# Kernel tuning notes

Measured on AMD Instinct MI355X. Metric: run time of the kernel, lower is better.

The kernel has to match this reference:

```python
import jax, jax.numpy as jnp
import numpy as np

H = 16      # query heads
KV = 8      # kv heads
D = 128     # head_dim
HID = 2048  # hidden_size
T = 2048    # tokens
EPS = 1e-6
THETA = 1000000.0


def setup_inputs() -> dict:
    key = jax.random.key(0)
    ks = jax.random.split(key, 4)
    return {
        "hidden_states": jax.random.normal(ks[0], (T, HID), jnp.float32),
        "positions": jnp.arange(T, dtype=jnp.int32),
        "qkv_w": jax.random.normal(ks[1], (H * D + 2 * KV * D, HID), jnp.float32) * 0.02,
        "o_w": jax.random.normal(ks[2], (HID, H * D), jnp.float32) * 0.02,
        "q_norm_w": jnp.ones((D,), jnp.float32),
        "k_norm_w": jnp.ones((D,), jnp.float32),
    }


def _rmsnorm(x, w):
    # x: [T, heads, D]; normalize over last dim
    var = jnp.mean(x * x, axis=-1, keepdims=True)
    return x * jax.lax.rsqrt(var + EPS) * w


def _rope(x, positions):
    # neox-style rotate-half; x: [T, heads, D]
    half = D // 2
    inv_freq = 1.0 / (THETA ** (jnp.arange(0, half, dtype=jnp.float32) / half * 1.0))
    inv_freq = 1.0 / (THETA ** (jnp.arange(0, D, 2, dtype=jnp.float32) / D))
    ang = positions.astype(jnp.float32)[:, None] * inv_freq  # [T, D/2]
    cos = jnp.cos(ang)[:, None, :]
    sin = jnp.sin(ang)[:, None, :]
    x1, x2 = x[..., :half], x[..., half:]
    return jnp.concatenate([x1 * cos - x2 * sin, x2 * cos + x1 * sin], axis=-1)


def reference(hidden_states, positions, qkv_w, o_w, q_norm_w, k_norm_w):
    scale = D ** -0.5
    qkv = hidden_states @ qkv_w.T  # [T, H*D + 2*KV*D]
    q = qkv[:, : H * D].reshape(T, H, D)
    k = qkv[:, H * D : H * D + KV * D].reshape(T, KV, D)
    v = qkv[:, H * D + KV * D :].reshape(T, KV, D)

    q = _rope(_rmsnorm(q, q_norm_w), positions)
    k = _rope(_rmsnorm(k, k_norm_w), positions)

    # GQA: repeat kv heads to match query heads
    rep = H // KV
    k = jnp.repeat(k, rep, axis=1)  # [T, H, D]
    v = jnp.repeat(v, rep, axis=1)

    scores = jnp.einsum("thd,shd->hts", q, k) * scale  # [H, T, T]
    causal = positions[:, None] >= positions[None, :]  # [T, T]
    scores = jnp.where(causal[None, :, :], scores, jnp.float32(-1e30))
    p = jax.nn.softmax(scores, axis=-1)
    o = jnp.einsum("hts,shd->thd", p, v).reshape(T, H * D)
    return o @ o_w.T  # [T, HID]
```

## Files before the change

kernel.cpp:

```cpp
#include <hip/hip_runtime.h>
#include <math.h>

#define T_TOK 2048
#define HID 2048
#define NH 16
#define NKV 8
#define HD 128
#define QKV_N 4096
#define EPS 1e-6f

typedef unsigned short u16;
typedef unsigned int   u32;
typedef __attribute__((ext_vector_type(8))) u16   u16x8;
typedef __attribute__((ext_vector_type(8))) short short8;
typedef __attribute__((ext_vector_type(4))) float floatx4;
typedef __attribute__((ext_vector_type(16))) float f32x16;
typedef __attribute__((ext_vector_type(4))) u32   u32x4;

__device__ __forceinline__ u16 f2bf(float x) {
    u32 u = __float_as_uint(x);
    u = (u + 0x7fffu + ((u >> 16) & 1u)) >> 16;
    return (u16)u;
}
__device__ __forceinline__ float bf2f(u16 h) {
    return __uint_as_float(((u32)h) << 16);
}
__device__ __forceinline__ u32 cvtpk_bf16(float lo, float hi) {
    u32 r;
    asm("v_cvt_pk_bf16_f32 %0, %1, %2" : "=v"(r) : "v"(lo), "v"(hi));
    return r;
}

__device__ __forceinline__ void cvt8(const float* __restrict__ in,
                                     u16* __restrict__ out, size_t i)
{
    float4 a = *(const float4*)(in + i);
    float4 b = *(const float4*)(in + i + 4);
    u16x8 o;
    o[0] = f2bf(a.x); o[1] = f2bf(a.y); o[2] = f2bf(a.z); o[3] = f2bf(a.w);
    o[4] = f2bf(b.x); o[5] = f2bf(b.y); o[6] = f2bf(b.z); o[7] = f2bf(b.w);
    *(u16x8*)(out + i) = o;
}

__global__ __launch_bounds__(256) void cvt_pair(
    const float* __restrict__ ina, u16* __restrict__ outa,
    const float* __restrict__ inb, u16* __restrict__ outb)
{
    const int bid = blockIdx.x;
    if (bid < 2048) cvt8(ina, outa, ((size_t)bid * 256 + threadIdx.x) * 8);
    else            cvt8(inb, outb, ((size_t)(bid - 2048) * 256 + threadIdx.x) * 8);
}

__global__ __launch_bounds__(256) void addf32(
    float* __restrict__ out, const float* __restrict__ part)
{
    const size_t i = ((size_t)blockIdx.x * 256 + threadIdx.x) * 8;
    float4 a0 = *(const float4*)(out + i);
    float4 a1 = *(const float4*)(out + i + 4);
    float4 b0 = *(const float4*)(part + i);
    float4 b1 = *(const float4*)(part + i + 4);
    a0.x += b0.x; a0.y += b0.y; a0.z += b0.z; a0.w += b0.w;
    a1.x += b1.x; a1.y += b1.y; a1.z += b1.z; a1.w += b1.w;
    *(float4*)(out + i)     = a0;
    *(float4*)(out + i + 4) = a1;
}

#define GBM 256
#define GBN 128
#define GBK 64
#define BUFSH 24576

#define WAITV6 asm volatile("s_waitcnt vmcnt(6)" ::: "memory")
#define WAITV0 asm volatile("s_waitcnt vmcnt(0)" ::: "memory")
#define LGKM0  asm volatile("s_waitcnt lgkmcnt(0)" ::: "memory")
#define BARR   asm volatile("s_barrier" ::: "memory")
#define SB     __builtin_amdgcn_sched_barrier(0)

#define STAGEU(i, tt, dstb) \
    __builtin_amdgcn_global_load_lds( \
        (const __attribute__((address_space(1))) u32*)(gsrc[i] + (size_t)(tt)*GBK), \
        (__attribute__((address_space(3))) u32*)((dstb) + loff[i]), 16, 0, 0)

#define RD_A(dst, srcb, f) do { \
    dst[0] = *(const short8*)((srcb) + arow + (f)*1024 + achunk0); \
    dst[1] = *(const short8*)((srcb) + arow + (f)*1024 + achunk1); } while (0)

#define RD_B(dst, srcb) do { \
    _Pragma("unroll") \
    for (int j_ = 0; j_ < 4; ++j_) { \
        dst[j_][0] = *(const short8*)((srcb) + 16384 + brow + j_*1024 + achunk0); \
        dst[j_][1] = *(const short8*)((srcb) + 16384 + brow + j_*1024 + achunk1); } } while (0)

#define MM(f, aa, bb) do { \
    __builtin_amdgcn_s_setprio(1); \
    _Pragma("unroll") \
    for (int j_ = 0; j_ < 4; ++j_) { \
        acc[f][j_] = __builtin_amdgcn_mfma_f32_16x16x32_bf16(aa[0], bb[j_][0], acc[f][j_], 0, 0, 0); \
        acc[f][j_] = __builtin_amdgcn_mfma_f32_16x16x32_bf16(aa[1], bb[j_][1], acc[f][j_], 0, 0, 0); } \
    __builtin_amdgcn_s_setprio(0); } while (0)

#define TILE(t, CURB, NXTB, THDB, BBC, BBN) do { \
    const bool st_ = (t) + 2 < nt; \
    if (st_) { STAGEU(0, (t)+2, THDB); STAGEU(1, (t)+2, THDB); } \
    RD_A(aP1, CURB, 1); SB; \
    MM(0, aP0, BBC); SB; \
    if (st_) { STAGEU(2, (t)+2, THDB); STAGEU(3, (t)+2, THDB); } \
    RD_A(aP0, CURB, 2); SB; \
    MM(1, aP1, BBC); SB; \
    if (st_) { STAGEU(4, (t)+2, THDB); STAGEU(5, (t)+2, THDB); } \
    RD_A(aP1, CURB, 3); SB; \
    MM(2, aP0, BBC); \
    if ((t) + 1 < nt) { \
        if (st_) { WAITV6; } else { WAITV0; } \
        LGKM0; BARR; SB; \
        RD_B(BBN, NXTB); RD_A(aP0, NXTB, 0); \
    } \
    SB; \
    MM(3, aP1, BBC); SB; \
} while (0)

template<bool OUT_BF16>
__global__ __launch_bounds__(512, 2) void gemm_bt_8p(
    const u16* __restrict__ A, const u16* __restrict__ B,
    void* __restrict__ Cv, void* __restrict__ Cv2,
    int Ks, int lda, int ldb, int ldc)
{
    extern __shared__ short lds[];
    const int tid = threadIdx.x;
    const int w  = tid >> 6;
    const int l  = tid & 63;
    const int m0 = blockIdx.y * GBM;
    const int n0 = blockIdx.x * GBN;
    const int z  = blockIdx.z;
    A += (size_t)z * Ks;
    B += (size_t)z * Ks;
    void* Cw = z ? Cv2 : Cv;
    const int mr = (w >> 1) * 64;
    const int nc = (w & 1) * 64;
    const int cc = l & 15;
    const int q4 = l >> 4;

    const int lr = l >> 3;
    const int gchunk = ((l & 7) ^ (lr & 7)) * 8;
    const u16* gsrc[6]; int loff[6];
    #pragma unroll
    for (int i = 0; i < 6; ++i) {
        const int u = w * 6 + i;
        if (u < 32) {
            gsrc[i] = A + (size_t)(m0 + u*8 + lr) * lda + gchunk;
            loff[i] = u * 512;
        } else {
            const int v = u - 32;
            gsrc[i] = B + (size_t)(n0 + v*8 + lr) * ldb + gchunk;
            loff[i] = 16384 + v * 512;
        }
    }

    const int achunk0 = ((q4)     ^ (cc & 7)) * 8;
    const int achunk1 = ((4 + q4) ^ (cc & 7)) * 8;
    const int arow = (mr + cc) * 64;
    const int brow = (nc + cc) * 64;

    floatx4 acc[4][4];
    #pragma unroll
    for (int f = 0; f < 4; ++f)
        #pragma unroll
        for (int j = 0; j < 4; ++j) acc[f][j] = (floatx4){0.f, 0.f, 0.f, 0.f};

    short8 aP0[2], aP1[2], bbE[4][2], bbO[4][2];
    short* b0 = lds;
    short* b1 = lds + BUFSH;
    short* b2 = lds + 2 * BUFSH;
    const int nt = Ks >> 6;

    #pragma unroll
    for (int i = 0; i < 6; ++i) STAGEU(i, 0, b0);
    #pragma unroll
    for (int i = 0; i < 6; ++i) STAGEU(i, 1, b1);
    WAITV6; BARR; SB;
    RD_B(bbE, b0); RD_A(aP0, b0, 0);

    short *CURB = b0, *NXTB = b1, *THDB = b2;
    for (int t = 0; t < nt; t += 2) {
        TILE(t, CURB, NXTB, THDB, bbE, bbO);
        { short* tmp = CURB; CURB = NXTB; NXTB = THDB; THDB = tmp; }
        TILE(t + 1, CURB, NXTB, THDB, bbO, bbE);
        { short* tmp = CURB; CURB = NXTB; NXTB = THDB; THDB = tmp; }
    }

    const int r0 = q4 * 4;
    #pragma unroll
    for (int f = 0; f < 4; ++f)
        #pragma unroll
        for (int j = 0; j < 4; ++j)
            #pragma unroll
            for (int r = 0; r < 4; ++r) {
                const int row = m0 + mr + f*16 + r0 + r;
                const int col = n0 + nc + j*16 + cc;
                if (OUT_BF16)
                    ((u16*)Cw)[(size_t)row * ldc + col] = f2bf(acc[f][j][r]);
                else
                    ((float*)Cw)[(size_t)row * ldc + col] = acc[f][j][r];
            }
}

__global__ __launch_bounds__(256) void prep_cvt(
    u16* __restrict__ qkv, const int* __restrict__ positions,
    const float* __restrict__ qw, const float* __restrict__ kw,
    u16* __restrict__ Kp, u16* __restrict__ Vtp,
    const float* __restrict__ ow, u16* __restrict__ owbf)
{
    const int bid = blockIdx.x;
    if (bid >= 256) {
        cvt8(ow, owbf, ((size_t)(bid - 256) * 256 + threadIdx.x) * 8);
        return;
    }
    const int tile = bid & 31, kvh = bid >> 5;
    const int tid = threadIdx.x;
    const int w = tid >> 6, l = tid & 63;
    const int t0 = tile * 64;

    const float qw0 = qw[2*l], qw1 = qw[2*l+1];
    const float kw0 = kw[2*l], kw1 = kw[2*l+1];
    const int   i0  = (2*l) & 63;
    const float if0 = exp2f(-(float)i0     * 0.311430758895690f);
    const float if1 = exp2f(-(float)(i0+1) * 0.311430758895690f);

    for (int rr = w; rr < 64; rr += 4) {
        const int t = t0 + rr;
        const int pos = positions[t];
        const float a0 = (float)pos * if0;
        const float a1 = (float)pos * if1;
        const float s0 = sinf(a0), c0 = cosf(a0);
        const float s1 = sinf(a1), c1 = cosf(a1);

        #pragma unroll
        for (int pass = 0; pass < 3; ++pass) {
            const int off = (pass < 2) ? (2*kvh + pass)*HD : NH*HD + kvh*HD;
            const float w0 = (pass < 2) ? qw0 : kw0;
            const float w1 = (pass < 2) ? qw1 : kw1;
            u16* p = qkv + (size_t)t*QKV_N + off;

            const u32 pk = *(const u32*)(p + 2*l);
            const float x0 = bf2f((u16)pk), x1 = bf2f((u16)(pk >> 16));
            float ss = x0*x0 + x1*x1;
            #pragma unroll
            for (int x = 1; x < 64; x <<= 1) ss += __shfl_xor(ss, x);
            const float rs = rsqrtf(ss * (1.0f/128.0f) + EPS);
            const float xn0 = x0 * rs * w0, xn1 = x1 * rs * w1;
            const float px0 = __shfl_xor(xn0, 32);
            const float px1 = __shfl_xor(xn1, 32);

            float o0, o1;
            if (l < 32) { o0 = xn0*c0 - px0*s0; o1 = xn1*c1 - px1*s1; }
            else        { o0 = xn0*c0 + px0*s0; o1 = xn1*c1 + px1*s1; }
            const u32 outpk = (u32)f2bf(o0) | ((u32)f2bf(o1) << 16);

            if (pass < 2) {
                *(u32*)(p + 2*l) = outpk;
            } else {
                const int ch = l >> 2;
                u16* dst = Kp + ((size_t)(kvh*32 + tile)*64 + rr)*128
                              + (ch ^ (rr & 15))*8 + (l & 3)*2;
                *(u32*)dst = outpk;
            }
        }
    }

    __shared__ u16 tl[64][136];
    {
        const int t  = tid >> 2;
        const int c0 = (tid & 3) * 32;
        const u16* src = qkv + (size_t)(t0 + t)*QKV_N + NH*HD + NKV*HD + kvh*HD + c0;
        #pragma unroll
        for (int p2 = 0; p2 < 4; ++p2)
            *(u16x8*)(&tl[t][c0 + p2*8]) = *(const u16x8*)(src + p2*8);
    }
    __syncthreads();
    {
        u16* dstb = Vtp + (size_t)(kvh*32 + tile) * 128 * 64;
        #pragma unroll
        for (int i = 0; i < 4; ++i) {
            const int id = tid*4 + i;
            const int d = id >> 3;
            const int o = id & 7;
            const int sb = (o ^ (d & 7)) * 8;
            u16x8 v;
            #pragma unroll
            for (int j = 0; j < 8; ++j) v[j] = tl[sb + j][d];
            *(u16x8*)(dstb + d*64 + o*8) = v;
        }
    }
}

__global__ __launch_bounds__(256, 2) void attn_mfma32(
    const u16* __restrict__ qkv, const u16* __restrict__ Kp,
    const u16* __restrict__ Vtp,
    u16* __restrict__ Opart, float2* __restrict__ ml)
{
    const int id   = blockIdx.x;
    const int kvh  = id & 7;
    const int u    = id >> 3;
    const int half = u >> 5;
    const int v    = u & 31;
    const int hp   = v & 1;
    const int bq   = v >> 1;
    const int qt   = half ? bq : 15 - bq;
    const int h    = kvh*2 + hp;
    const int t0q  = qt * 128;

    const int tid = threadIdx.x;
    const int w   = tid >> 6;
    const int l   = tid & 63;
    const int q31 = l & 31;
    const int hi  = l >> 5;

    __shared__ short Ks[2][8192];
    __shared__ short Vts[2][8192];

    short8 qf[8];
    {
        const u16* qrow = qkv + (size_t)(t0q + w*32 + q31) * QKV_N + h*HD;
        #pragma unroll
        for (int ks = 0; ks < 8; ++ks)
            qf[ks] = *(const short8*)(qrow + ks*16 + hi*8);
    }

    float m_run = -3.0e38f, l_run = 0.f;
    f32x16 accO[4];
    #pragma unroll
    for (int nd = 0; nd < 4; ++nd)
        #pragma unroll
        for (int r = 0; r < 16; ++r) accO[nd][r] = 0.f;

    const float Cs = 0.12751744f;

    const int nt  = 2*qt + 2;
    const int nh0 = qt + 1;
    const int tlo = half ? nh0 : 0;
    const int thi = half ? nt  : nh0;

    auto issue = [&](int tile, int buf) {
        const size_t tb = (size_t)(kvh*32 + tile) * 8192;
        const u16* g = ((w < 2) ? Kp : Vtp) + tb + (w & 1)*4096 + l*8;
        short* p = ((w < 2) ? Ks[buf] : Vts[buf]) + (w & 1)*4096 + l*8;
        #pragma unroll
        for (int i = 0; i < 8; ++i)
            __builtin_amdgcn_global_load_lds(
                (const __attribute__((address_space(1))) u32*)(g + i*512),
                (__attribute__((address_space(3))) u32*)(p + i*512), 16, 0, 0);
    };

    issue(tlo, 0);
    int cur = 0;

    for (int tile = tlo; tile < thi; ++tile) {
        __syncthreads();
        if (tile + 1 < thi) issue(tile + 1, cur ^ 1);

        const short* Kc = Ks[cur];
        const short* Vc = Vts[cur];

        f32x16 accS0, accS1;
        #pragma unroll
        for (int r = 0; r < 16; ++r) { accS0[r] = 0.f; accS1[r] = 0.f; }

        __builtin_amdgcn_s_setprio(1);
        #pragma unroll
        for (int ks = 0; ks < 8; ++ks) {
            const int pc = ((2*ks + hi) ^ (q31 & 15)) * 8;
            short8 a0 = *(const short8*)(Kc + q31*128 + pc);
            short8 a1 = *(const short8*)(Kc + (32 + q31)*128 + pc);
            accS0 = __builtin_amdgcn_mfma_f32_32x32x16_bf16(a0, qf[ks], accS0, 0, 0, 0);
            accS1 = __builtin_amdgcn_mfma_f32_32x32x16_bf16(a1, qf[ks], accS1, 0, 0, 0);
        }
        __builtin_amdgcn_s_setprio(0);

        if (tile >= 2*qt) {
            const int qg = w*32 + q31 + t0q - tile*64;
            #pragma unroll
            for (int r = 0; r < 16; ++r) {
                const int kvb = (r&3) + 8*(r>>2) + (hi<<2);
                if (kvb > qg)      accS0[r] = -1.0e30f;
                if (kvb + 32 > qg) accS1[r] = -1.0e30f;
            }
        }

        float mx = accS0[0];
        #pragma unroll
        for (int r = 1; r < 16; ++r) mx = fmaxf(mx, accS0[r]);
        #pragma unroll
        for (int r = 0; r < 16; ++r) mx = fmaxf(mx, accS1[r]);
        mx = fmaxf(mx, __shfl_xor(mx, 32));

        if (__any(mx > m_run + 11.76f)) {
            const float m_new = fmaxf(m_run, mx);
            const float alpha = exp2f((m_run - m_new) * Cs);
            l_run *= alpha;
            m_run = m_new;
            #pragma unroll
            for (int r = 0; r < 16; ++r) {
                const float ar = __shfl(alpha, ((r&3) + 8*(r>>2)) + (hi<<2));
                accO[0][r] *= ar; accO[1][r] *= ar;
                accO[2][r] *= ar; accO[3][r] *= ar;
            }
        }

        const float mb = m_run * Cs;
        float lsum = 0.f;
        #pragma unroll
        for (int r = 0; r < 16; ++r) {
            const float e0 = exp2f(accS0[r]*Cs - mb);
            const float e1 = exp2f(accS1[r]*Cs - mb);
            accS0[r] = e0; accS1[r] = e1;
            lsum += e0 + e1;
        }
        lsum += __shfl_xor(lsum, 32);
        l_run += lsum;

        __builtin_amdgcn_s_setprio(1);
        #pragma unroll
        for (int ks = 0; ks < 4; ++ks) {
            const int R = (ks & 1) * 8;
            u32 x0, x1, x2, x3;
            if (ks < 2) {
                x0 = cvtpk_bf16(accS0[R+0], accS0[R+1]);
                x1 = cvtpk_bf16(accS0[R+2], accS0[R+3]);
                x2 = cvtpk_bf16(accS0[R+4], accS0[R+5]);
                x3 = cvtpk_bf16(accS0[R+6], accS0[R+7]);
            } else {
                x0 = cvtpk_bf16(accS1[R+0], accS1[R+1]);
                x1 = cvtpk_bf16(accS1[R+2], accS1[R+3]);
                x2 = cvtpk_bf16(accS1[R+4], accS1[R+5]);
                x3 = cvtpk_bf16(accS1[R+6], accS1[R+7]);
            }
            asm("v_permlane32_swap_b32 %0, %1" : "+v"(x0), "+v"(x2));
            asm("v_permlane32_swap_b32 %0, %1" : "+v"(x1), "+v"(x3));
            u32x4 aw; aw.x = x0; aw.y = x1; aw.z = x2; aw.w = x3;
            const short8 aP = __builtin_bit_cast(short8, aw);
            #pragma unroll
            for (int nd = 0; nd < 4; ++nd) {
                short8 bv = *(const short8*)(Vc + (nd*32 + q31)*64
                                             + ((2*ks + hi) ^ (q31 & 7))*8);
                accO[nd] = __builtin_amdgcn_mfma_f32_32x32x16_bf16(aP, bv, accO[nd], 0, 0, 0);
            }
        }
        __builtin_amdgcn_s_setprio(0);

        cur ^= 1;
    }

    const size_t pbase = (size_t)(half * NH + h) * T_TOK;
    #pragma unroll
    for (int r = 0; r < 16; ++r) {
        const int qr = (r&3) + 8*(r>>2) + (hi<<2);
        u16* op = Opart + (pbase + t0q + w*32 + qr) * HD;
        op[q31]      = f2bf(accO[0][r]);
        op[32 + q31] = f2bf(accO[1][r]);
        op[64 + q31] = f2bf(accO[2][r]);
        op[96 + q31] = f2bf(accO[3][r]);
    }
    if (l < 32)
        ml[pbase + t0q + w*32 + l] = make_float2(m_run, l_run);
}

__global__ __launch_bounds__(256) void attn_combine(
    const u16* __restrict__ Opart, const float2* __restrict__ ml,
    u16* __restrict__ qkv)
{
    const int idx = blockIdx.x * 256 + threadIdx.x;
    const int c16 = idx & 15;
    const int t   = (idx >> 4) & (T_TOK - 1);
    const int h   = idx >> 15;
    const size_t iA = (size_t)h * T_TOK + t;
    const size_t iB = (size_t)(NH + h) * T_TOK + t;
    const float2 a = ml[iA];
    const float2 b = ml[iB];
    const float Cs = 0.12751744f;
    const float mM = fmaxf(a.x, b.x);
    const float wA = exp2f((a.x - mM) * Cs);
    const float wB = exp2f((b.x - mM) * Cs);
    const float inv = 1.0f / (wA * a.y + wB * b.y);
    const u16x8 A = *(const u16x8*)(Opart + iA * HD + c16*8);
    const u16x8 B = *(const u16x8*)(Opart + iB * HD + c16*8);
    u16x8 o;
    #pragma unroll
    for (int j = 0; j < 8; ++j)
        o[j] = f2bf((wA * bf2f(A[j]) + wB * bf2f(B[j])) * inv);
    *(u16x8*)(qkv + (size_t)t * QKV_N + h * HD + c16*8) = o;
}

extern "C" void kernel_launch(void* const* d_in, const int* in_sizes, int n_in,
                              void* d_out, int out_size, void* d_ws, size_t ws_size,
                              hipStream_t stream)
{
    const float* hidden    = (const float*)d_in[0];
    const int*   positions = (const int*)  d_in[1];
    const float* qkv_w     = (const float*)d_in[2];
    const float* o_w       = (const float*)d_in[3];
    const float* q_norm_w  = (const float*)d_in[4];
    const float* k_norm_w  = (const float*)d_in[5];
    float* out = (float*)d_out;

    u16* qkvbf = (u16*)d_ws;
    u16* wbf   = qkvbf + (size_t)T_TOK * QKV_N;
    u16* abf   = wbf   + (size_t)QKV_N * HID;
    u16* kpb   = abf   + (size_t)T_TOK * HID;
    u16* vpb   = kpb   + (size_t)NKV * T_TOK * HD;
    float* partC = (float*)wbf;

    static bool s_attr = false;
    if (!s_attr) {
        (void)hipFuncSetAttribute(
            reinterpret_cast<const void*>(&gemm_bt_8p<true>),
            hipFuncAttributeMaxDynamicSharedMemorySize, 147456);
        (void)hipFuncSetAttribute(
            reinterpret_cast<const void*>(&gemm_bt_8p<false>),
            hipFuncAttributeMaxDynamicSharedMemorySize, 147456);
        s_attr = true;
    }

    cvt_pair<<<6144, 256, 0, stream>>>(hidden, abf, qkv_w, wbf);

    gemm_bt_8p<true><<<dim3(QKV_N/GBN, T_TOK/GBM, 1), 512, 147456, stream>>>(
        abf, wbf, qkvbf, qkvbf, HID, HID, HID, QKV_N);

    prep_cvt<<<2304, 256, 0, stream>>>(
        qkvbf, positions, q_norm_w, k_norm_w, kpb, vpb, o_w, abf);

    attn_mfma32<<<512, 256, 0, stream>>>(qkvbf, kpb, vpb, wbf, (float2*)out);

    attn_combine<<<(NH*T_TOK*16)/256, 256, 0, stream>>>(
        wbf, (const float2*)out, qkvbf);

    gemm_bt_8p<false><<<dim3(HID/GBN, T_TOK/GBM, 2), 512, 147456, stream>>>(
        qkvbf, abf, out, partC, HID/2, QKV_N, HID, HID);

    addf32<<<(T_TOK*HID)/2048, 256, 0, stream>>>(out, partC);
}
```

Before: 244.5 us.

## Split attention KV range four ways with 512-thread blocks and move o_w conversion

```diff
diff --git a/kernel.cpp b/kernel.cpp
--- a/kernel.cpp
+++ b/kernel.cpp
@@ -204,17 +204,12 @@
             }
 }
 
-__global__ __launch_bounds__(256) void prep_cvt(
+__global__ __launch_bounds__(256) void prep(
     u16* __restrict__ qkv, const int* __restrict__ positions,
     const float* __restrict__ qw, const float* __restrict__ kw,
-    u16* __restrict__ Kp, u16* __restrict__ Vtp,
-    const float* __restrict__ ow, u16* __restrict__ owbf)
+    u16* __restrict__ Kp, u16* __restrict__ Vtp)
 {
     const int bid = blockIdx.x;
-    if (bid >= 256) {
-        cvt8(ow, owbf, ((size_t)(bid - 256) * 256 + threadIdx.x) * 8);
-        return;
-    }
     const int tile = bid & 31, kvh = bid >> 5;
     const int tid = threadIdx.x;
     const int w = tid >> 6, l = tid & 63;
@@ -293,21 +288,23 @@
     }
 }
 
-__global__ __launch_bounds__(256, 2) void attn_mfma32(
+__global__ __launch_bounds__(512, 4) void attn_mfma32(
     const u16* __restrict__ qkv, const u16* __restrict__ Kp,
     const u16* __restrict__ Vtp,
-    u16* __restrict__ Opart, float2* __restrict__ ml)
-{
-    const int id   = blockIdx.x;
-    const int kvh  = id & 7;
-    const int u    = id >> 3;
-    const int half = u >> 5;
-    const int v    = u & 31;
-    const int hp   = v & 1;
-    const int bq   = v >> 1;
-    const int qt   = half ? bq : 15 - bq;
-    const int h    = kvh*2 + hp;
-    const int t0q  = qt * 128;
+    u16* __restrict__ P0, u16* __restrict__ P1,
+    u16* __restrict__ P2, u16* __restrict__ P3,
+    float2* __restrict__ ml)
+{
+    const int id  = blockIdx.x;
+    const int kvh = id & 7;
+    const int u   = id >> 3;
+    const int hp  = u & 1;
+    const int p   = (u >> 1) & 3;
+    const int q3  = (u >> 3) & 3;
+    const int top = u >> 5;
+    const int qt  = top ? 7 - q3 : q3;
+    const int h   = kvh*2 + hp;
+    const int t0q = qt * 256;
 
     const int tid = threadIdx.x;
     const int w   = tid >> 6;
@@ -335,20 +332,19 @@
 
     const float Cs = 0.12751744f;
 
-    const int nt  = 2*qt + 2;
-    const int nh0 = qt + 1;
-    const int tlo = half ? nh0 : 0;
-    const int thi = half ? nt  : nh0;
+    const int nt  = 4*qt + 4;
+    const int tlo = p * (qt + 1);
+    const int thi = tlo + (qt + 1);
 
     auto issue = [&](int tile, int buf) {
         const size_t tb = (size_t)(kvh*32 + tile) * 8192;
-        const u16* g = ((w < 2) ? Kp : Vtp) + tb + (w & 1)*4096 + l*8;
-        short* p = ((w < 2) ? Ks[buf] : Vts[buf]) + (w & 1)*4096 + l*8;
-        #pragma unroll
-        for (int i = 0; i < 8; ++i)
+        const u16* g = ((w < 4) ? Kp : Vtp) + tb + (w & 3)*2048 + l*8;
+        short* pl = ((w < 4) ? Ks[buf] : Vts[buf]) + (w & 3)*2048 + l*8;
+        #pragma unroll
+        for (int i = 0; i < 4; ++i)
             __builtin_amdgcn_global_load_lds(
                 (const __attribute__((address_space(1))) u32*)(g + i*512),
-                (__attribute__((address_space(3))) u32*)(p + i*512), 16, 0, 0);
+                (__attribute__((address_space(3))) u32*)(pl + i*512), 16, 0, 0);
     };
 
     issue(tlo, 0);
@@ -376,13 +372,14 @@
         }
         __builtin_amdgcn_s_setprio(0);
 
-        if (tile >= 2*qt) {
-            const int qg = w*32 + q31 + t0q - tile*64;
+        if (tile >= 4*qt) {
+            const int qg   = t0q + w*32 + q31;
+            const int kvb0 = tile*64 + (hi << 2);
             #pragma unroll
             for (int r = 0; r < 16; ++r) {
-                const int kvb = (r&3) + 8*(r>>2) + (hi<<2);
-                if (kvb > qg)      accS0[r] = -1.0e30f;
-                if (kvb + 32 > qg) accS1[r] = -1.0e30f;
+                const int kvg = kvb0 + (r&3) + 8*(r>>2);
+                if (kvg > qg)      accS0[r] = -1.0e30f;
+                if (kvg + 32 > qg) accS1[r] = -1.0e30f;
             }
         }
 
@@ -450,43 +447,58 @@
         cur ^= 1;
     }
 
-    const size_t pbase = (size_t)(half * NH + h) * T_TOK;
+    u16* Op = (p == 0) ? P0 : (p == 1) ? P1 : (p == 2) ? P2 : P3;
+    const size_t hb = (size_t)h * T_TOK;
     #pragma unroll
     for (int r = 0; r < 16; ++r) {
         const int qr = (r&3) + 8*(r>>2) + (hi<<2);
-        u16* op = Opart + (pbase + t0q + w*32 + qr) * HD;
+        u16* op = Op + (hb + t0q + w*32 + qr) * HD;
         op[q31]      = f2bf(accO[0][r]);
         op[32 + q31] = f2bf(accO[1][r]);
         op[64 + q31] = f2bf(accO[2][r]);
         op[96 + q31] = f2bf(accO[3][r]);
     }
     if (l < 32)
-        ml[pbase + t0q + w*32 + l] = make_float2(m_run, l_run);
-}
-
-__global__ __launch_bounds__(256) void attn_combine(
-    const u16* __restrict__ Opart, const float2* __restrict__ ml,
-    u16* __restrict__ qkv)
-{
-    const int idx = blockIdx.x * 256 + threadIdx.x;
+        ml[(size_t)p*NH*T_TOK + hb + t0q + w*32 + l]
+            = make_float2(m_run, l_run);
+}
+
+__global__ __launch_bounds__(256) void combine4_cvt(
+    const u16* __restrict__ P0, const u16* __restrict__ P1,
+    const u16* __restrict__ P2, const u16* __restrict__ P3,
+    const float2* __restrict__ ml, u16* __restrict__ qkv,
+    const float* __restrict__ ow, u16* __restrict__ owbf)
+{
+    const int bid = blockIdx.x;
+    if (bid >= 2048) {
+        cvt8(ow, owbf, ((size_t)(bid - 2048) * 256 + threadIdx.x) * 8);
+        return;
+    }
+    const int idx = bid * 256 + threadIdx.x;
     const int c16 = idx & 15;
     const int t   = (idx >> 4) & (T_TOK - 1);
     const int h   = idx >> 15;
-    const size_t iA = (size_t)h * T_TOK + t;
-    const size_t iB = (size_t)(NH + h) * T_TOK + t;
-    const float2 a = ml[iA];
-    const float2 b = ml[iB];
+    const size_t base = (size_t)h * T_TOK + t;
+    const size_t NT = (size_t)NH * T_TOK;
+    const float2 a = ml[base];
+    const float2 b = ml[base + NT];
+    const float2 c = ml[base + 2*NT];
+    const float2 d = ml[base + 3*NT];
     const float Cs = 0.12751744f;
-    const float mM = fmaxf(a.x, b.x);
+    const float mM = fmaxf(fmaxf(a.x, b.x), fmaxf(c.x, d.x));
     const float wA = exp2f((a.x - mM) * Cs);
     const float wB = exp2f((b.x - mM) * Cs);
-    const float inv = 1.0f / (wA * a.y + wB * b.y);
-    const u16x8 A = *(const u16x8*)(Opart + iA * HD + c16*8);
-    const u16x8 B = *(const u16x8*)(Opart + iB * HD + c16*8);
+    const float wC = exp2f((c.x - mM) * Cs);
+    const float wD = exp2f((d.x - mM) * Cs);
+    const float inv = 1.0f / (wA*a.y + wB*b.y + wC*c.y + wD*d.y);
+    const u16x8 A = *(const u16x8*)(P0 + base * HD + c16*8);
+    const u16x8 B = *(const u16x8*)(P1 + base * HD + c16*8);
+    const u16x8 C = *(const u16x8*)(P2 + base * HD + c16*8);
+    const u16x8 D = *(const u16x8*)(P3 + base * HD + c16*8);
     u16x8 o;
     #pragma unroll
     for (int j = 0; j < 8; ++j)
-        o[j] = f2bf((wA * bf2f(A[j]) + wB * bf2f(B[j])) * inv);
+        o[j] = f2bf((wA*bf2f(A[j]) + wB*bf2f(B[j]) + wC*bf2f(C[j]) + wD*bf2f(D[j])) * inv);
     *(u16x8*)(qkv + (size_t)t * QKV_N + h * HD + c16*8) = o;
 }
 
@@ -507,6 +519,12 @@
     u16* abf   = wbf   + (size_t)QKV_N * HID;
     u16* kpb   = abf   + (size_t)T_TOK * HID;
     u16* vpb   = kpb   + (size_t)NKV * T_TOK * HD;
+
+    u16* P0 = wbf;
+    u16* P1 = wbf + (size_t)NH * T_TOK * HD;
+    u16* P2 = abf;
+    u16* P3 = (u16*)out;
+    float2* mlp = (float2*)((u16*)out + (size_t)NH * T_TOK * HD);
     float* partC = (float*)wbf;
 
     static bool s_attr = false;
@@ -525,16 +543,14 @@
     gemm_bt_8p<true><<<dim3(QKV_N/GBN, T_TOK/GBM, 1), 512, 147456, stream>>>(
         abf, wbf, qkvbf, qkvbf, HID, HID, HID, QKV_N);
 
-    prep_cvt<<<2304, 256, 0, stream>>>(
-        qkvbf, positions, q_norm_w, k_norm_w, kpb, vpb, o_w, abf);
-
-    attn_mfma32<<<512, 256, 0, stream>>>(qkvbf, kpb, vpb, wbf, (float2*)out);
-
-    attn_combine<<<(NH*T_TOK*16)/256, 256, 0, stream>>>(
-        wbf, (const float2*)out, qkvbf);
+    prep<<<256, 256, 0, stream>>>(qkvbf, positions, q_norm_w, k_norm_w, kpb, vpb);
+
+    attn_mfma32<<<512, 512, 0, stream>>>(qkvbf, kpb, vpb, P0, P1, P2, P3, mlp);
+
+    combine4_cvt<<<4096, 256, 0, stream>>>(P0, P1, P2, P3, mlp, qkvbf, o_w, kpb);
 
     gemm_bt_8p<false><<<dim3(HID/GBN, T_TOK/GBM, 2), 512, 147456, stream>>>(
-        qkvbf, abf, out, partC, HID/2, QKV_N, HID, HID);
+        qkvbf, kpb, out, partC, HID/2, QKV_N, HID, HID);
 
     addf32<<<(T_TOK*HID)/2048, 256, 0, stream>>>(out, partC);
 }
```

Result: slower. 282.2 us (+15.4%).
